# Performance work log

Measured on AMD Instinct MI355X. Metric: run time of the kernel, lower is better.

Reference implementation:

```python
import jax, jax.numpy as jnp
import numpy as np

EMBED_DIM = 1024
NUM_HEADS = 16
HEAD_DIM = EMBED_DIM // NUM_HEADS


def setup_inputs() -> dict:
    key = jax.random.key(0)
    ks = jax.random.split(key, 6)
    s = 1.0 / np.sqrt(EMBED_DIM)
    return {
        "x": jax.random.normal(ks[0], (4, 2048, EMBED_DIM), dtype=jnp.float32),
        "Wq": jax.random.uniform(ks[1], (EMBED_DIM, EMBED_DIM), jnp.float32, -s, s),
        "Wk": jax.random.uniform(ks[2], (EMBED_DIM, EMBED_DIM), jnp.float32, -s, s),
        "Wv": jax.random.uniform(ks[3], (EMBED_DIM, EMBED_DIM), jnp.float32, -s, s),
        "Wo": jax.random.uniform(ks[4], (EMBED_DIM, EMBED_DIM), jnp.float32, -s, s),
        "bo": jax.random.uniform(ks[5], (EMBED_DIM,), jnp.float32, -s, s),
    }


def reference(x, Wq, Wk, Wv, Wo, bo):
    B, S, E = x.shape
    H, D = NUM_HEADS, HEAD_DIM
    # torch Linear: x @ W.T ; reshape to [B, H, S, D]
    q = (x @ Wq.T).reshape(B, S, H, D).transpose(0, 2, 1, 3)
    k = (x @ Wk.T).reshape(B, S, H, D).transpose(0, 2, 1, 3)
    v = (x @ Wv.T).reshape(B, S, H, D).transpose(0, 2, 1, 3)
    scores = jnp.einsum("bhqd,bhkd->bhqk", q, k) / jnp.sqrt(jnp.float32(D))
    attn = jax.nn.softmax(scores, axis=-1)  # dropout is identity in eval mode
    out = jnp.einsum("bhqk,bhkd->bhqd", attn, v)
    out = out.transpose(0, 2, 1, 3).reshape(B, S, E)
    return out @ Wo.T + bo
```

## Files before the change

kernel.cpp:

```cpp
#include <hip/hip_runtime.h>
#include <hip/hip_bf16.h>
#include <math.h>

#define B_ 4
#define S_ 2048
#define E_ 1024
#define H_ 16
#define D_ 64
#define M_ (B_*S_)
#define NKV 32

typedef __attribute__((ext_vector_type(8))) short short8;
typedef __attribute__((ext_vector_type(4))) short short4_t;
typedef __attribute__((ext_vector_type(4))) float f32x4;
typedef __attribute__((ext_vector_type(16))) float f32x16;

static __device__ __forceinline__ short f2bf(float f){
  union { float f; unsigned u; } v; v.f = f;
  unsigned u = v.u + 0x7FFFu + ((v.u >> 16) & 1u);
  return (short)(u >> 16);
}

__global__ void cast_all(const float* __restrict__ x,
    const float* __restrict__ wq, const float* __restrict__ wk,
    const float* __restrict__ wv, const float* __restrict__ wo,
    short8* __restrict__ xb, short8* __restrict__ wqb, short8* __restrict__ wkb,
    short8* __restrict__ wvb, short8* __restrict__ wob){
  int bid = blockIdx.x;
  const float* src; short8* dst; int i;
  if (bid < 4096) { src = x; dst = xb; i = bid*256 + threadIdx.x; }
  else {
    int k = (bid - 4096) >> 9;
    i = ((bid - 4096) & 511)*256 + threadIdx.x;
    src = k==0 ? wq : k==1 ? wk : k==2 ? wv : wo;
    dst = k==0 ? wqb : k==1 ? wkb : k==2 ? wvb : wob;
  }
  const float4* s4 = (const float4*)src;
  float4 a = s4[2*i], b = s4[2*i+1];
  short8 o;
  o[0]=f2bf(a.x); o[1]=f2bf(a.y); o[2]=f2bf(a.z); o[3]=f2bf(a.w);
  o[4]=f2bf(b.x); o[5]=f2bf(b.y); o[6]=f2bf(b.z); o[7]=f2bf(b.w);
  dst[i]=o;
}

#define GLOAD16(g, l) __builtin_amdgcn_global_load_lds( \
    (const __attribute__((address_space(1))) void*)(g), \
    (__attribute__((address_space(3))) void*)(l), 16, 0, 0)

__global__ __launch_bounds__(256,2) void gemm_qkv(const short* __restrict__ A,
      const short* __restrict__ Wf, short* __restrict__ Qo, short* __restrict__ Ko,
      short* __restrict__ Vto, float u)
{
  __shared__ short AL[128*32];
  __shared__ short BL[128*32];
  const int tid = threadIdx.x;
  const int w = tid >> 6, lane = tid & 63;
  const int l15 = lane & 15, l4 = lane >> 4;
  const int m0 = blockIdx.x * 128;
  const int n0 = blockIdx.y * 128;
  const int wr = w >> 1, wc = w & 1;
  f32x4 acc[4][4] = {};

  const short* ga = A  + (size_t)(m0 + (tid>>2))*1024 + (tid&3)*8;
  const short* gb = Wf + (size_t)(n0 + (tid>>2))*1024 + (tid&3)*8;

  for (int kt = 0; kt < 32; ++kt) {
    const int ko = kt*32;
    #pragma unroll
    for (int p = 0; p < 2; ++p) {
      GLOAD16(ga + (size_t)(p*64)*1024 + ko, (char*)AL + p*4096 + w*1024);
      GLOAD16(gb + (size_t)(p*64)*1024 + ko, (char*)BL + p*4096 + w*1024);
    }
    __syncthreads();
    short8 af[4], bw[4];
    #pragma unroll
    for (int i = 0; i < 4; ++i) {
      af[i] = *(const short8*)(AL + (wr*64 + i*16 + l15)*32 + 8*l4);
      bw[i] = *(const short8*)(BL + (wc*64 + i*16 + l15)*32 + 8*l4);
    }
    #pragma unroll
    for (int i = 0; i < 4; ++i)
      #pragma unroll
      for (int j = 0; j < 4; ++j)
        acc[i][j] = __builtin_amdgcn_mfma_f32_16x16x32_bf16(af[i], bw[j], acc[i][j], 0,0,0);
    __syncthreads();
  }

  const int sel = n0 >> 10;
  const int nc0 = n0 & 1023;
  if (sel == 2) {
    #pragma unroll
    for (int i = 0; i < 4; ++i) {
      int row = m0 + wr*64 + i*16 + 4*l4;
      int b = row >> 11;
      int s0 = row & 2047;
      #pragma unroll
      for (int j = 0; j < 4; ++j) {
        int col = nc0 + wc*64 + j*16 + l15;
        int h = col >> 6, d = col & 63;
        short4_t pk;
        pk[0]=f2bf(acc[i][j][0]); pk[1]=f2bf(acc[i][j][1]);
        pk[2]=f2bf(acc[i][j][2]); pk[3]=f2bf(acc[i][j][3]);
        *(short4_t*)(Vto + (((size_t)(b*H_ + h))*D_ + d)*S_ + s0) = pk;
      }
    }
  } else {
    short* O = sel ? Ko : Qo;
    float sc = sel ? 1.0f : u;
    #pragma unroll
    for (int i = 0; i < 4; ++i) {
      int row = m0 + wr*64 + i*16 + 4*l4;
      int b = row >> 11;
      #pragma unroll
      for (int j = 0; j < 4; ++j) {
        int col = nc0 + wc*64 + j*16 + l15;
        int h = col >> 6, d = col & 63;
        #pragma unroll
        for (int r = 0; r < 4; ++r) {
          int s = (row + r) & 2047;
          O[(((size_t)(b*H_ + h))*S_ + s)*D_ + d] = f2bf(acc[i][j][r]*sc);
        }
      }
    }
  }
}

__global__ __launch_bounds__(256,2) void gemm_out(const short* __restrict__ A,
      const short* __restrict__ W, float* __restrict__ out,
      const float* __restrict__ bias)
{
  __shared__ short AL[128*32];
  __shared__ short BL[128*32];
  const int tid = threadIdx.x;
  const int w = tid >> 6, lane = tid & 63;
  const int l15 = lane & 15, l4 = lane >> 4;
  const int m0 = blockIdx.x * 128;
  const int n0 = blockIdx.y * 128;
  const int wr = w >> 1, wc = w & 1;
  f32x4 acc[4][4] = {};

  const short* ga = A + (size_t)(m0 + (tid>>2))*1024 + (tid&3)*8;
  const short* gb = W + (size_t)(n0 + (tid>>2))*1024 + (tid&3)*8;

  for (int kt = 0; kt < 32; ++kt) {
    const int ko = kt*32;
    #pragma unroll
    for (int p = 0; p < 2; ++p) {
      GLOAD16(ga + (size_t)(p*64)*1024 + ko, (char*)AL + p*4096 + w*1024);
      GLOAD16(gb + (size_t)(p*64)*1024 + ko, (char*)BL + p*4096 + w*1024);
    }
    __syncthreads();
    short8 af[4], bw[4];
    #pragma unroll
    for (int i = 0; i < 4; ++i) {
      af[i] = *(const short8*)(AL + (wr*64 + i*16 + l15)*32 + 8*l4);
      bw[i] = *(const short8*)(BL + (wc*64 + i*16 + l15)*32 + 8*l4);
    }
    #pragma unroll
    for (int i = 0; i < 4; ++i)
      #pragma unroll
      for (int j = 0; j < 4; ++j)
        acc[i][j] = __builtin_amdgcn_mfma_f32_16x16x32_bf16(af[i], bw[j], acc[i][j], 0,0,0);
    __syncthreads();
  }

  #pragma unroll
  for (int i = 0; i < 4; ++i) {
    int row = m0 + wr*64 + i*16 + 4*l4;
    #pragma unroll
    for (int j = 0; j < 4; ++j) {
      int col = n0 + wc*64 + j*16 + l15;
      float bz = bias[col];
      #pragma unroll
      for (int r = 0; r < 4; ++r)
        out[(size_t)(row + r)*1024 + col] = acc[i][j][r] + bz;
    }
  }
}

static __device__ __forceinline__ unsigned cvtpk(float lo, float hi){
  unsigned d; asm("v_cvt_pk_bf16_f32 %0, %1, %2" : "=v"(d) : "v"(lo), "v"(hi)); return d;
}
template<int BASE>
static __device__ __forceinline__ short8 pfrag(const f32x16 &s, int hi){
  unsigned w01 = cvtpk(s[BASE+0], s[BASE+1]);
  unsigned w23 = cvtpk(s[BASE+2], s[BASE+3]);
  unsigned w45 = cvtpk(s[BASE+4], s[BASE+5]);
  unsigned w67 = cvtpk(s[BASE+6], s[BASE+7]);
  unsigned x01=(unsigned)__shfl_xor((int)w01,32), x23=(unsigned)__shfl_xor((int)w23,32);
  unsigned x45=(unsigned)__shfl_xor((int)w45,32), x67=(unsigned)__shfl_xor((int)w67,32);
  union { unsigned u[4]; short8 s8; } r;
  r.u[0] = hi ? x45 : w01;
  r.u[1] = hi ? x67 : w23;
  r.u[2] = hi ? w45 : x01;
  r.u[3] = hi ? w67 : x23;
  return r.s8;
}

__global__ __launch_bounds__(256,4) void attn_kernel(const short* __restrict__ Qb,
    const short* __restrict__ Kb, const short* __restrict__ Vtb, short* __restrict__ Ob)
{
  __shared__ short KL[2][64*64];
  __shared__ short VL[2][64*64];
  const int tid = threadIdx.x, w = tid >> 6, lane = tid & 63;
  const int l31 = lane & 31, hi = lane >> 5;
  const int rx7 = l31 & 7;

  const int linear = blockIdx.x;
  const int swz = (linear & 7)*128 + (linear >> 3);
  const int bh = swz >> 4;
  const int b = bh >> 4, h = bh & 15;
  const int q0 = (swz & 15) * 128;

  const short* Qg = Qb + ((size_t)bh*S_ + q0)*D_;
  const short* Kg = Kb + (size_t)bh*S_*D_;
  const short* Vg = Vtb + (size_t)bh*D_*S_;

  const int srow = tid >> 3;
  const int scol = ((tid & 7) ^ (srow & 7)) * 8;

  #define STAGE(t, bi) { \
    GLOAD16(Kg + (size_t)((t)*64 +      srow)*D_ + scol, (char*)KL[bi] + w*1024); \
    GLOAD16(Kg + (size_t)((t)*64 + 32 + srow)*D_ + scol, (char*)KL[bi] + 4096 + w*1024); \
    GLOAD16(Vg + (size_t)(     srow)*S_ + (t)*64 + scol, (char*)VL[bi] + w*1024); \
    GLOAD16(Vg + (size_t)(32 + srow)*S_ + (t)*64 + scol, (char*)VL[bi] + 4096 + w*1024); }

  STAGE(0, 0)

  const int qrow = w*32 + l31;
  short8 qf[4];
  #pragma unroll
  for (int t = 0; t < 4; ++t)
    qf[t] = *(const short8*)(Qg + (size_t)qrow*D_ + (2*t + hi)*8);

  f32x16 oacc[2] = {};
  float l_run = 0.f;

  for (int kv = 0; kv < NKV; ++kv) {
    const int cur = kv & 1;
    if (kv < NKV-1) {
      STAGE(kv+1, cur^1)
      asm volatile("s_waitcnt vmcnt(4)" ::: "memory");
    } else {
      asm volatile("s_waitcnt vmcnt(0)" ::: "memory");
    }
    __builtin_amdgcn_s_barrier();
    asm volatile("" ::: "memory");
    __builtin_amdgcn_sched_barrier(0);

    f32x16 st[2] = {};
    __builtin_amdgcn_s_setprio(1);
    #pragma unroll
    for (int t = 0; t < 4; ++t) {
      int co = ((2*t + hi) ^ rx7)*16;
      short8 ka0 = *(const short8*)((char*)KL[cur] + l31*128 + co);
      short8 ka1 = *(const short8*)((char*)KL[cur] + (32 + l31)*128 + co);
      st[0] = __builtin_amdgcn_mfma_f32_32x32x16_bf16(ka0, qf[t], st[0], 0,0,0);
      st[1] = __builtin_amdgcn_mfma_f32_32x32x16_bf16(ka1, qf[t], st[1], 0,0,0);
    }
    __builtin_amdgcn_s_setprio(0);

    #pragma unroll
    for (int r = 0; r < 16; ++r) st[0][r] = __builtin_amdgcn_exp2f(st[0][r]);
    #pragma unroll
    for (int r = 0; r < 16; ++r) st[1][r] = __builtin_amdgcn_exp2f(st[1][r]);
    {
      f32x16 sv = st[0] + st[1];
      float sa = (sv[0]+sv[1]) + (sv[2]+sv[3]);
      float sb = (sv[4]+sv[5]) + (sv[6]+sv[7]);
      float sc = (sv[8]+sv[9]) + (sv[10]+sv[11]);
      float sd = (sv[12]+sv[13]) + (sv[14]+sv[15]);
      l_run += (sa+sb) + (sc+sd);
    }

    short8 pf[4];
    pf[0] = pfrag<0>(st[0], hi);
    pf[1] = pfrag<8>(st[0], hi);
    pf[2] = pfrag<0>(st[1], hi);
    pf[3] = pfrag<8>(st[1], hi);

    __builtin_amdgcn_s_setprio(1);
    #pragma unroll
    for (int t = 0; t < 4; ++t) {
      int co = ((2*t + hi) ^ rx7)*16;
      short8 va0 = *(const short8*)((char*)VL[cur] + l31*128 + co);
      short8 va1 = *(const short8*)((char*)VL[cur] + (32 + l31)*128 + co);
      oacc[0] = __builtin_amdgcn_mfma_f32_32x32x16_bf16(va0, pf[t], oacc[0], 0,0,0);
      oacc[1] = __builtin_amdgcn_mfma_f32_32x32x16_bf16(va1, pf[t], oacc[1], 0,0,0);
    }
    __builtin_amdgcn_s_setprio(0);
    __builtin_amdgcn_sched_barrier(0);
    asm volatile("" ::: "memory");
    __builtin_amdgcn_s_barrier();
    asm volatile("" ::: "memory");
  }
  #undef STAGE

  float lt = l_run + __shfl_xor(l_run, 32);
  float inv = 1.f / lt;
  int s = q0 + qrow;
  short* orow = Ob + ((size_t)(b*S_ + s))*E_ + h*64;
  #pragma unroll
  for (int r = 0; r < 16; r += 2) {
    int d0 = (r & 3) + 8*(r >> 2) + 4*hi;
    unsigned pa = (unsigned short)f2bf(oacc[0][r]*inv) |
                  ((unsigned)(unsigned short)f2bf(oacc[0][r+1]*inv) << 16);
    unsigned pb = (unsigned short)f2bf(oacc[1][r]*inv) |
                  ((unsigned)(unsigned short)f2bf(oacc[1][r+1]*inv) << 16);
    *(unsigned*)(orow + d0) = pa;
    *(unsigned*)(orow + 32 + d0) = pb;
  }
}

extern "C" void kernel_launch(void* const* d_in, const int* in_sizes, int n_in,
                              void* d_out, int out_size, void* d_ws, size_t ws_size,
                              hipStream_t stream) {
  const float* x  = (const float*)d_in[0];
  const float* Wq = (const float*)d_in[1];
  const float* Wk = (const float*)d_in[2];
  const float* Wv = (const float*)d_in[3];
  const float* Wo = (const float*)d_in[4];
  const float* bo = (const float*)d_in[5];

  char* ws = (char*)d_ws;
  short* xb  = (short*)(ws);
  short* Wqb = (short*)(ws + (16u<<20));
  short* Wkb = (short*)(ws + (18u<<20));
  short* Wvb = (short*)(ws + (20u<<20));
  short* Wob = (short*)(ws + (22u<<20));
  short* Qb  = (short*)(ws + (24u<<20));
  short* Kb  = (short*)(ws + (40u<<20));
  short* Vtb = (short*)(ws + (56u<<20));
  short* Ab  = (short*)(ws + (72u<<20));

  cast_all<<<4096 + 4*512, 256, 0, stream>>>(x, Wq, Wk, Wv, Wo,
      (short8*)xb, (short8*)Wqb, (short8*)Wkb, (short8*)Wvb, (short8*)Wob);

  const float u = 0.18033688011112042f;
  gemm_qkv<<<dim3(64, 24), 256, 0, stream>>>(xb, Wqb, Qb, Kb, Vtb, u);

  attn_kernel<<<1024, 256, 0, stream>>>(Qb, Kb, Vtb, Ab);

  gemm_out<<<dim3(64, 8), 256, 0, stream>>>(Ab, Wob, (float*)d_out, bo);
}
```

Baseline: 194.7 us.

## Swizzle GEMM block order and use permlane32 swap for P fragments

Remaps the linear block index in the QKV and output projection GEMMs to a swizzled order, spreading consecutive blocks across XCDs so tiles sharing A rows or W columns sit together in each L2. In the attention kernel, the four shfl_xor-by-32 exchanges plus selects that build the bf16 P fragments become two v_permlane32_swap instructions. The swap cuts cross-lane traffic and VALU selects on the softmax-to-PV path, but relies on the swap semantics matching the old half-wave exchange.

New measurement: 200.9 us. 3.2% more time.

```diff
diff --git a/kernel.cpp b/kernel.cpp
--- a/kernel.cpp
+++ b/kernel.cpp
@@ -56,8 +56,10 @@
   const int tid = threadIdx.x;
   const int w = tid >> 6, lane = tid & 63;
   const int l15 = lane & 15, l4 = lane >> 4;
-  const int m0 = blockIdx.x * 128;
-  const int n0 = blockIdx.y * 128;
+  const int linear = blockIdx.y * 64 + blockIdx.x;
+  const int swzb = (linear & 7)*192 + (linear >> 3);
+  const int m0 = (swzb & 63) * 128;
+  const int n0 = (swzb >> 6) * 128;
   const int wr = w >> 1, wc = w & 1;
   f32x4 acc[4][4] = {};
 
@@ -134,8 +136,10 @@
   const int tid = threadIdx.x;
   const int w = tid >> 6, lane = tid & 63;
   const int l15 = lane & 15, l4 = lane >> 4;
-  const int m0 = blockIdx.x * 128;
-  const int n0 = blockIdx.y * 128;
+  const int linear = blockIdx.y * 64 + blockIdx.x;
+  const int swzb = (linear & 7)*64 + (linear >> 3);
+  const int m0 = (swzb & 63) * 128;
+  const int n0 = (swzb >> 6) * 128;
   const int wr = w >> 1, wc = w & 1;
   f32x4 acc[4][4] = {};
 
@@ -181,19 +185,19 @@
 static __device__ __forceinline__ unsigned cvtpk(float lo, float hi){
   unsigned d; asm("v_cvt_pk_bf16_f32 %0, %1, %2" : "=v"(d) : "v"(lo), "v"(hi)); return d;
 }
+static __device__ __forceinline__ void plswap(unsigned &a, unsigned &b){
+  asm("v_permlane32_swap_b32 %0, %1" : "+v"(a), "+v"(b));
+}
 template<int BASE>
-static __device__ __forceinline__ short8 pfrag(const f32x16 &s, int hi){
+static __device__ __forceinline__ short8 pfrag(const f32x16 &s){
   unsigned w01 = cvtpk(s[BASE+0], s[BASE+1]);
   unsigned w23 = cvtpk(s[BASE+2], s[BASE+3]);
   unsigned w45 = cvtpk(s[BASE+4], s[BASE+5]);
   unsigned w67 = cvtpk(s[BASE+6], s[BASE+7]);
-  unsigned x01=(unsigned)__shfl_xor((int)w01,32), x23=(unsigned)__shfl_xor((int)w23,32);
-  unsigned x45=(unsigned)__shfl_xor((int)w45,32), x67=(unsigned)__shfl_xor((int)w67,32);
+  plswap(w01, w45);
+  plswap(w23, w67);
   union { unsigned u[4]; short8 s8; } r;
-  r.u[0] = hi ? x45 : w01;
-  r.u[1] = hi ? x67 : w23;
-  r.u[2] = hi ? w45 : x01;
-  r.u[3] = hi ? w67 : x23;
+  r.u[0]=w01; r.u[1]=w23; r.u[2]=w45; r.u[3]=w67;
   return r.s8;
 }
 
@@ -274,10 +278,10 @@
     }
 
     short8 pf[4];
-    pf[0] = pfrag<0>(st[0], hi);
-    pf[1] = pfrag<8>(st[0], hi);
-    pf[2] = pfrag<0>(st[1], hi);
-    pf[3] = pfrag<8>(st[1], hi);
+    pf[0] = pfrag<0>(st[0]);
+    pf[1] = pfrag<8>(st[0]);
+    pf[2] = pfrag<0>(st[1]);
+    pf[3] = pfrag<8>(st[1]);
 
     __builtin_amdgcn_s_setprio(1);
     #pragma unroll
```
